# Kernel tuning notes

Measured on AMD Instinct MI355X. Metric: run time of the kernel, lower is better.

The kernel has to match this reference:

```python
import jax, jax.numpy as jnp
import numpy as np

N = 50000
E = 800000
DIM_IN = 128
DIM_H = 16
HEADS = 8
DIM_OUT = 16
NEG_SLOPE = 0.2


def setup_inputs() -> dict:
    key = jax.random.key(0)
    ks = jax.random.split(key, 12)
    def glorot(k, shape):
        fan_in = shape[0]
        return jax.random.normal(k, shape, dtype=jnp.float32) / np.sqrt(fan_in)
    x = jax.random.normal(ks[0], (N, DIM_IN), dtype=jnp.float32)
    edge_index = jax.random.randint(ks[1], (2, E), 0, N, dtype=jnp.int64)
    # layer 1: GATv2Conv(dim_in, dim_h, heads=8)
    Wl1 = glorot(ks[2], (DIM_IN, HEADS * DIM_H))
    Wr1 = glorot(ks[3], (DIM_IN, HEADS * DIM_H))
    att1 = glorot(ks[4], (HEADS, DIM_H))
    bias1 = jnp.zeros((HEADS * DIM_H,), dtype=jnp.float32)
    # layer 2: GATv2Conv(dim_h*heads, dim_out, heads=1)
    Wl2 = glorot(ks[5], (HEADS * DIM_H, DIM_OUT))
    Wr2 = glorot(ks[6], (HEADS * DIM_H, DIM_OUT))
    att2 = glorot(ks[7], (1, DIM_OUT))
    bias2 = jnp.zeros((DIM_OUT,), dtype=jnp.float32)
    return {"x": x, "edge_index": edge_index, "Wl1": Wl1, "Wr1": Wr1,
            "att1": att1, "bias1": bias1, "Wl2": Wl2, "Wr2": Wr2,
            "att2": att2, "bias2": bias2}


def gatv2_layer(x, src, dst, Wl, Wr, att, bias, n_nodes, heads, ch):
    # x: [N, F_in]; src/dst: [Etot] (self-loops included)
    xl = (x @ Wl).reshape(n_nodes, heads, ch)  # source transform
    xr = (x @ Wr).reshape(n_nodes, heads, ch)  # target transform
    e = jax.nn.leaky_relu(xl[src] + xr[dst], NEG_SLOPE)      # [Etot, H, C]
    logits = jnp.einsum('ehc,hc->eh', e, att)                # [Etot, H]
    # segment softmax over incoming edges of each target node
    m = jax.ops.segment_max(logits, dst, num_segments=n_nodes)
    a = jnp.exp(logits - m[dst])
    denom = jax.ops.segment_sum(a, dst, num_segments=n_nodes)
    alpha = a / denom[dst]                                   # [Etot, H]
    out = jax.ops.segment_sum(xl[src] * alpha[:, :, None], dst,
                              num_segments=n_nodes)          # [N, H, C]
    return out.reshape(n_nodes, heads * ch) + bias


def reference(x, edge_index, Wl1, Wr1, att1, bias1, Wl2, Wr2, att2, bias2):
    # PyG GATv2Conv adds self-loops by default
    loops = jnp.arange(N, dtype=edge_index.dtype)
    src = jnp.concatenate([edge_index[0], loops])
    dst = jnp.concatenate([edge_index[1], loops])
    # dropout is identity in eval mode
    h = gatv2_layer(x, src, dst, Wl1, Wr1, att1, bias1, N, HEADS, DIM_H)
    h = jax.nn.elu(h)
    h = gatv2_layer(h, src, dst, Wl2, Wr2, att2, bias2, N, 1, DIM_OUT)
    return h, jax.nn.log_softmax(h, axis=1)
```

## Files before the change

### kernel.cpp

```cpp
#include <hip/hip_runtime.h>
#include <hip/hip_bf16.h>
#include <math.h>

#define NN 50000
#define EE 800000
#define DIN 128
#define HEADS 8
#define DH 16
#define DOUT 16
#define NEG 0.2f
#define GM 32
#define GB ((NN + GM - 1) / GM)
#define NB ((NN + 255) / 256)
#define DEGB ((EE / 4 + 255) / 256)
#define NPART 8
#define RANGE (NN / NPART)
#define FILLB (DEGB * NPART)
#define PAD 64

typedef __attribute__((ext_vector_type(8))) short bf16x8;
typedef __attribute__((ext_vector_type(4))) float f32x4;
typedef __attribute__((ext_vector_type(4))) int i32x4;

__device__ __forceinline__ unsigned pack2bf(float a, float b) {
    union { __hip_bfloat162 h; unsigned u; } c;
    c.h = __float22bfloat162_rn(make_float2(a, b));
    return c.u;
}
__device__ __forceinline__ unsigned short f2bf(float v) {
    union { __hip_bfloat16 h; unsigned short u; } c;
    c.h = __float2bfloat16(v);
    return c.u;
}
__device__ __forceinline__ float bflo(unsigned u) { return __uint_as_float(u << 16); }
__device__ __forceinline__ float bfhi(unsigned u) { return __uint_as_float(u & 0xffff0000u); }

__global__ __launch_bounds__(256) void init_wcvt(int* __restrict__ cnt,
                                                 unsigned short* __restrict__ esrcPad,
                                                 const float* __restrict__ Wl,
                                                 const float* __restrict__ Wr,
                                                 unsigned short* __restrict__ Wb,
                                                 const float* __restrict__ Wl2,
                                                 const float* __restrict__ Wr2,
                                                 unsigned short* __restrict__ Wb2) {
    int b = blockIdx.x, t = threadIdx.x;
    if (b < NB) {
        int i = b * 256 + t;
        if (i < NN) {
            cnt[i] = 1;
            esrcPad[(size_t)i * PAD] = (unsigned short)i;
        }
    } else if (b < NB + 128) {
        int i = (b - NB) * 256 + t;
        int n = i >> 7, k = i & 127;
        float v = (n < 128) ? Wl[k * 128 + n] : Wr[k * 128 + (n - 128)];
        Wb[i] = f2bf(v);
    } else {
        int i = (b - NB - 128) * 256 + t;
        int n = i >> 7, k = i & 127;
        float v = (n < 16) ? Wl2[k * 16 + n] : Wr2[k * 16 + (n - 16)];
        Wb2[i] = f2bf(v);
    }
}

__global__ __launch_bounds__(256) void fill_gemm1(const int* __restrict__ ei,
                                                  int* __restrict__ cnt,
                                                  unsigned short* __restrict__ esrcPad,
                                                  const float* __restrict__ x,
                                                  const unsigned short* __restrict__ Wb,
                                                  unsigned short* __restrict__ xlb,
                                                  float* __restrict__ xr) {
    __shared__ unsigned short As[GM][136];
    int t = threadIdx.x;
    if (blockIdx.x < FILLB) {
        int chunk = blockIdx.x >> 3;
        int r = blockIdx.x & 7;
        int i = chunk * 256 + t;
        if (i >= EE / 4) return;
        i32x4 ss = __builtin_nontemporal_load(((const i32x4*)ei) + i);
        i32x4 dd = __builtin_nontemporal_load(((const i32x4*)(ei + EE)) + i);
        int lo = r * RANGE;
        int p;
        if ((unsigned)(dd[0] - lo) < RANGE) {
            p = atomicAdd(&cnt[dd[0]], 1);
            esrcPad[(size_t)dd[0] * PAD + p] = (unsigned short)ss[0];
        }
        if ((unsigned)(dd[1] - lo) < RANGE) {
            p = atomicAdd(&cnt[dd[1]], 1);
            esrcPad[(size_t)dd[1] * PAD + p] = (unsigned short)ss[1];
        }
        if ((unsigned)(dd[2] - lo) < RANGE) {
            p = atomicAdd(&cnt[dd[2]], 1);
            esrcPad[(size_t)dd[2] * PAD + p] = (unsigned short)ss[2];
        }
        if ((unsigned)(dd[3] - lo) < RANGE) {
            p = atomicAdd(&cnt[dd[3]], 1);
            esrcPad[(size_t)dd[3] * PAD + p] = (unsigned short)ss[3];
        }
        return;
    }
    int n0 = (blockIdx.x - FILLB) * GM;
    {
        int row = t >> 3, seg = t & 7;
        int nsrc = n0 + row < NN ? n0 + row : NN - 1;
        const f32x4* xp = (const f32x4*)(x + (size_t)nsrc * DIN + 16 * seg);
        f32x4 v0 = __builtin_nontemporal_load(xp);
        f32x4 v1 = __builtin_nontemporal_load(xp + 1);
        f32x4 v2 = __builtin_nontemporal_load(xp + 2);
        f32x4 v3 = __builtin_nontemporal_load(xp + 3);
        uint4 p0 = make_uint4(pack2bf(v0[0], v0[1]), pack2bf(v0[2], v0[3]),
                              pack2bf(v1[0], v1[1]), pack2bf(v1[2], v1[3]));
        uint4 p1 = make_uint4(pack2bf(v2[0], v2[1]), pack2bf(v2[2], v2[3]),
                              pack2bf(v3[0], v3[1]), pack2bf(v3[2], v3[3]));
        *(uint4*)&As[row][16 * seg]     = p0;
        *(uint4*)&As[row][16 * seg + 8] = p1;
    }
    __syncthreads();
    int lane = t & 63, w = t >> 6;
    int m = lane & 15, quad = lane >> 4;
    f32x4 acc[2][4];
#pragma unroll
    for (int mt = 0; mt < 2; ++mt)
#pragma unroll
        for (int nt = 0; nt < 4; ++nt) acc[mt][nt] = (f32x4){0.f, 0.f, 0.f, 0.f};
#pragma unroll
    for (int ks = 0; ks < 4; ++ks) {
        int k = 32 * ks + 8 * quad;
        bf16x8 a0 = *(const bf16x8*)&As[m][k];
        bf16x8 a1 = *(const bf16x8*)&As[16 + m][k];
#pragma unroll
        for (int nt = 0; nt < 4; ++nt) {
            int n = 64 * w + 16 * nt + m;
            bf16x8 b = *(const bf16x8*)(Wb + (size_t)n * 128 + k);
            acc[0][nt] = __builtin_amdgcn_mfma_f32_16x16x32_bf16(a0, b, acc[0][nt], 0, 0, 0);
            acc[1][nt] = __builtin_amdgcn_mfma_f32_16x16x32_bf16(a1, b, acc[1][nt], 0, 0, 0);
        }
    }
#pragma unroll
    for (int mt = 0; mt < 2; ++mt) {
#pragma unroll
        for (int nt = 0; nt < 4; ++nt) {
            int col = 64 * w + 16 * nt + m;
            int rbase = n0 + 16 * mt + 4 * quad;
            if (col < 128) {
#pragma unroll
                for (int r = 0; r < 4; ++r) {
                    int row = rbase + r;
                    if (row < NN) xlb[(size_t)row * DIN + col] = f2bf(acc[mt][nt][r]);
                }
            } else {
#pragma unroll
                for (int r = 0; r < 4; ++r) {
                    int row = rbase + r;
                    if (row < NN)
                        __builtin_nontemporal_store(acc[mt][nt][r],
                                                    &xr[(size_t)row * DIN + (col - 128)]);
                }
            }
        }
    }
}

__global__ __launch_bounds__(256) void l1_fused(const unsigned short* __restrict__ esrcPad,
                                                const int* __restrict__ cnt,
                                                const unsigned short* __restrict__ xlb,
                                                const float* __restrict__ xr,
                                                const float* __restrict__ att,
                                                const float* __restrict__ bias,
                                                unsigned short* __restrict__ hb) {
    int d = blockIdx.x * 4 + (threadIdx.x >> 6);
    int lane = threadIdx.x & 63;
    int quarter = lane >> 4;
    int q16 = lane & 15;
    int rs = d * PAD;
    int re = rs + cnt[d];
    int last = re - 1;
    float4 xr0 = ((const float4*)(xr + (size_t)d * DIN))[2 * q16];
    float4 xr1 = ((const float4*)(xr + (size_t)d * DIN))[2 * q16 + 1];
    float4 at0 = ((const float4*)att)[2 * q16];
    float4 at1 = ((const float4*)att)[2 * q16 + 1];
    float4 a0 = make_float4(0.f, 0.f, 0.f, 0.f);
    float4 a1 = make_float4(0.f, 0.f, 0.f, 0.f);
    float l = 0.f;
    int slot = rs + quarter;
    int c0 = slot < last ? slot : last;
    int s0 = esrcPad[c0];
    int c1 = slot + 4 < last ? slot + 4 : last;
    int s1 = esrcPad[c1];
    uint4 row = ((const uint4*)(xlb + (size_t)s0 * DIN))[q16];
    for (; slot < re; slot += 4) {
        uint4 cur = row;
        int c2 = slot + 8 < last ? slot + 8 : last;
        int s2 = esrcPad[c2];
        row = ((const uint4*)(xlb + (size_t)s1 * DIN))[q16];
        s1 = s2;
        float f0 = bflo(cur.x), f1 = bfhi(cur.x);
        float f2 = bflo(cur.y), f3 = bfhi(cur.y);
        float f4 = bflo(cur.z), f5 = bfhi(cur.z);
        float f6 = bflo(cur.w), f7 = bfhi(cur.w);
        float v0 = f0 + xr0.x; v0 = fmaxf(v0, NEG * v0);
        float v1 = f1 + xr0.y; v1 = fmaxf(v1, NEG * v1);
        float v2 = f2 + xr0.z; v2 = fmaxf(v2, NEG * v2);
        float v3 = f3 + xr0.w; v3 = fmaxf(v3, NEG * v3);
        float v4 = f4 + xr1.x; v4 = fmaxf(v4, NEG * v4);
        float v5 = f5 + xr1.y; v5 = fmaxf(v5, NEG * v5);
        float v6 = f6 + xr1.z; v6 = fmaxf(v6, NEG * v6);
        float v7 = f7 + xr1.w; v7 = fmaxf(v7, NEG * v7);
        float w = at0.x * v0 + at0.y * v1 + at0.z * v2 + at0.w * v3
                + at1.x * v4 + at1.y * v5 + at1.z * v6 + at1.w * v7;
        w += __shfl_xor(w, 1);
        float p = __expf(w);
        a0.x += p * f0; a0.y += p * f1; a0.z += p * f2; a0.w += p * f3;
        a1.x += p * f4; a1.y += p * f5; a1.z += p * f6; a1.w += p * f7;
        l += p;
    }
#pragma unroll
    for (int off = 16; off < 64; off <<= 1) {
        a0.x += __shfl_xor(a0.x, off); a0.y += __shfl_xor(a0.y, off);
        a0.z += __shfl_xor(a0.z, off); a0.w += __shfl_xor(a0.w, off);
        a1.x += __shfl_xor(a1.x, off); a1.y += __shfl_xor(a1.y, off);
        a1.z += __shfl_xor(a1.z, off); a1.w += __shfl_xor(a1.w, off);
        l += __shfl_xor(l, off);
    }
    if (quarter == 0) {
        float inv = 1.f / l;
        float4 b0 = ((const float4*)bias)[2 * q16];
        float4 b1 = ((const float4*)bias)[2 * q16 + 1];
        float4 o0, o1;
        o0.x = a0.x * inv + b0.x; o0.x = o0.x > 0.f ? o0.x : expm1f(o0.x);
        o0.y = a0.y * inv + b0.y; o0.y = o0.y > 0.f ? o0.y : expm1f(o0.y);
        o0.z = a0.z * inv + b0.z; o0.z = o0.z > 0.f ? o0.z : expm1f(o0.z);
        o0.w = a0.w * inv + b0.w; o0.w = o0.w > 0.f ? o0.w : expm1f(o0.w);
        o1.x = a1.x * inv + b1.x; o1.x = o1.x > 0.f ? o1.x : expm1f(o1.x);
        o1.y = a1.y * inv + b1.y; o1.y = o1.y > 0.f ? o1.y : expm1f(o1.y);
        o1.z = a1.z * inv + b1.z; o1.z = o1.z > 0.f ? o1.z : expm1f(o1.z);
        o1.w = a1.w * inv + b1.w; o1.w = o1.w > 0.f ? o1.w : expm1f(o1.w);
        uint4 pk = make_uint4(pack2bf(o0.x, o0.y), pack2bf(o0.z, o0.w),
                              pack2bf(o1.x, o1.y), pack2bf(o1.z, o1.w));
        ((uint4*)(hb + (size_t)d * DIN))[q16] = pk;
    }
}

__global__ __launch_bounds__(256) void gemm2(const unsigned short* __restrict__ hb,
                                             const unsigned short* __restrict__ Wb2,
                                             float* __restrict__ xl2, float* __restrict__ xr2) {
    __shared__ unsigned short As[GM][136];
    int t = threadIdx.x;
    int n0 = blockIdx.x * GM;
    {
        int row = t >> 3, s8 = t & 7;
        int nsrc = n0 + row < NN ? n0 + row : NN - 1;
        const uint4* src = (const uint4*)(hb + (size_t)nsrc * DIN);
        *(uint4*)&As[row][8 * s8]      = src[s8];
        *(uint4*)&As[row][8 * s8 + 64] = src[s8 + 8];
    }
    __syncthreads();
    int lane = t & 63, w = t >> 6;
    int m = lane & 15, quad = lane >> 4;
    int mt = w & 1, nt = w >> 1;
    f32x4 acc = (f32x4){0.f, 0.f, 0.f, 0.f};
#pragma unroll
    for (int ks = 0; ks < 4; ++ks) {
        int k = 32 * ks + 8 * quad;
        bf16x8 a = *(const bf16x8*)&As[16 * mt + m][k];
        bf16x8 b = *(const bf16x8*)(Wb2 + (size_t)(16 * nt + m) * 128 + k);
        acc = __builtin_amdgcn_mfma_f32_16x16x32_bf16(a, b, acc, 0, 0, 0);
    }
    float* __restrict__ dst = (nt == 0) ? xl2 : xr2;
#pragma unroll
    for (int r = 0; r < 4; ++r) {
        int node = n0 + 16 * mt + 4 * quad + r;
        if (node < NN) dst[(size_t)node * DOUT + m] = acc[r];
    }
}

__global__ __launch_bounds__(256) void l2_fused(const unsigned short* __restrict__ esrcPad,
                                                const int* __restrict__ cnt,
                                                const float* __restrict__ xl,
                                                const float* __restrict__ xr,
                                                const float* __restrict__ att,
                                                const float* __restrict__ bias,
                                                float* __restrict__ out) {
    int d = blockIdx.x * 4 + (threadIdx.x >> 6);
    int lane = threadIdx.x & 63;
    int sl = lane >> 2;
    int q = lane & 3;
    int rs = d * PAD;
    int re = rs + cnt[d];
    int last = re - 1;
    float4 xrq = ((const float4*)(xr + (size_t)d * DOUT))[q];
    float4 atq = ((const float4*)att)[q];
    float4 acc = make_float4(0.f, 0.f, 0.f, 0.f);
    float l = 0.f;
    int slot = rs + sl;
    int c0 = slot < last ? slot : last;
    int s0 = esrcPad[c0];
    for (; slot < re; slot += 16) {
        int c1 = slot + 16 < last ? slot + 16 : last;
        int s1 = esrcPad[c1];
        float4 cur = ((const float4*)(xl + (size_t)s0 * DOUT))[q];
        s0 = s1;
        float v0 = cur.x + xrq.x; v0 = fmaxf(v0, NEG * v0);
        float v1 = cur.y + xrq.y; v1 = fmaxf(v1, NEG * v1);
        float v2 = cur.z + xrq.z; v2 = fmaxf(v2, NEG * v2);
        float v3 = cur.w + xrq.w; v3 = fmaxf(v3, NEG * v3);
        float w = atq.x * v0 + atq.y * v1 + atq.z * v2 + atq.w * v3;
        w += __shfl_xor(w, 1);
        w += __shfl_xor(w, 2);
        float p = __expf(w);
        acc.x += p * cur.x; acc.y += p * cur.y;
        acc.z += p * cur.z; acc.w += p * cur.w;
        l += p;
    }
#pragma unroll
    for (int off = 4; off < 64; off <<= 1) {
        acc.x += __shfl_xor(acc.x, off);
        acc.y += __shfl_xor(acc.y, off);
        acc.z += __shfl_xor(acc.z, off);
        acc.w += __shfl_xor(acc.w, off);
        l += __shfl_xor(l, off);
    }
    float inv = 1.f / l;
    float4 b = ((const float4*)bias)[q];
    float4 v;
    v.x = acc.x * inv + b.x; v.y = acc.y * inv + b.y;
    v.z = acc.z * inv + b.z; v.w = acc.w * inv + b.w;
    float m = fmaxf(fmaxf(v.x, v.y), fmaxf(v.z, v.w));
    m = fmaxf(m, __shfl_xor(m, 1));
    m = fmaxf(m, __shfl_xor(m, 2));
    float es = __expf(v.x - m) + __expf(v.y - m) + __expf(v.z - m) + __expf(v.w - m);
    es += __shfl_xor(es, 1);
    es += __shfl_xor(es, 2);
    float lse = m + __logf(es);
    if (sl == 0) {
        ((float4*)(out + (size_t)d * DOUT))[q] = v;
        float4 ls;
        ls.x = v.x - lse; ls.y = v.y - lse; ls.z = v.z - lse; ls.w = v.w - lse;
        ((float4*)(out + (size_t)NN * DOUT + (size_t)d * DOUT))[q] = ls;
    }
}

extern "C" void kernel_launch(void* const* d_in, const int* in_sizes, int n_in,
                              void* d_out, int out_size, void* d_ws, size_t ws_size,
                              hipStream_t stream) {
    const float* x     = (const float*)d_in[0];
    const int*   ei    = (const int*)d_in[1];
    const float* Wl1   = (const float*)d_in[2];
    const float* Wr1   = (const float*)d_in[3];
    const float* att1  = (const float*)d_in[4];
    const float* bias1 = (const float*)d_in[5];
    const float* Wl2   = (const float*)d_in[6];
    const float* Wr2   = (const float*)d_in[7];
    const float* att2  = (const float*)d_in[8];
    const float* bias2 = (const float*)d_in[9];
    float* out = (float*)d_out;

    float* xr1    = (float*)d_ws;
    float* xl2    = xr1 + (size_t)NN * DIN;
    float* xr2    = xl2 + (size_t)NN * DOUT;
    unsigned short* xlb = (unsigned short*)(xr2 + (size_t)NN * DOUT);
    unsigned short* hb  = xlb + (size_t)NN * DIN;
    unsigned short* Wb  = hb + (size_t)NN * DIN;
    unsigned short* Wb2 = Wb + 256 * 128;
    unsigned short* esrcPad = Wb2 + 32 * 128;
    int*   cnt    = (int*)(esrcPad + (size_t)NN * PAD);

    const int B = 256;
    init_wcvt<<<NB + 144, B, 0, stream>>>(cnt, esrcPad, Wl1, Wr1, Wb, Wl2, Wr2, Wb2);
    fill_gemm1<<<FILLB + GB, B, 0, stream>>>(ei, cnt, esrcPad, x, Wb, xlb, xr1);

    l1_fused<<<NN / 4, B, 0, stream>>>(esrcPad, cnt, xlb, xr1, att1, bias1, hb);

    gemm2<<<GB, B, 0, stream>>>(hb, Wb2, xl2, xr2);

    l2_fused<<<NN / 4, B, 0, stream>>>(esrcPad, cnt, xl2, xr2, att2, bias2, out);
}
```

Baseline: 237.9 us.

## Store layer-1 features head-major and split aggregation per head

Layer-1 source and target features, and the hidden output, are now stored head-major ([head][node][16]) instead of node-major. The aggregation kernel launches one block group per head, so each wave handles 8 edges at a time with 8 lanes per edge, and each gathered row is only 32 bytes per head. The likely aim is to shrink each gathered working set to one head's slice so it fits better in cache, and to raise parallelism. In exchange, every edge index is read eight times, the gathers are narrower, and gemm2 must reassemble rows from eight separate head planes.

```diff
diff --git a/kernel.cpp b/kernel.cpp
--- a/kernel.cpp
+++ b/kernel.cpp
@@ -20,6 +20,7 @@
 
 typedef __attribute__((ext_vector_type(8))) short bf16x8;
 typedef __attribute__((ext_vector_type(4))) float f32x4;
+typedef __attribute__((ext_vector_type(2))) float f32x2;
 typedef __attribute__((ext_vector_type(4))) int i32x4;
 
 __device__ __forceinline__ unsigned pack2bf(float a, float b) {
@@ -140,21 +141,24 @@
     for (int mt = 0; mt < 2; ++mt) {
 #pragma unroll
         for (int nt = 0; nt < 4; ++nt) {
-            int col = 64 * w + 16 * nt + m;
             int rbase = n0 + 16 * mt + 4 * quad;
-            if (col < 128) {
+            if (w < 2) {
+                int h = 4 * w + nt;
 #pragma unroll
                 for (int r = 0; r < 4; ++r) {
                     int row = rbase + r;
-                    if (row < NN) xlb[(size_t)row * DIN + col] = f2bf(acc[mt][nt][r]);
+                    if (row < NN)
+                        __builtin_nontemporal_store(f2bf(acc[mt][nt][r]),
+                            &xlb[((size_t)h * NN + row) * 16 + m]);
                 }
             } else {
+                int h = 4 * (w - 2) + nt;
 #pragma unroll
                 for (int r = 0; r < 4; ++r) {
                     int row = rbase + r;
                     if (row < NN)
                         __builtin_nontemporal_store(acc[mt][nt][r],
-                                                    &xr[(size_t)row * DIN + (col - 128)]);
+                            &xr[((size_t)h * NN + row) * 16 + m]);
                 }
             }
         }
@@ -168,76 +172,49 @@
                                                 const float* __restrict__ att,
                                                 const float* __restrict__ bias,
                                                 unsigned short* __restrict__ hb) {
-    int d = blockIdx.x * 4 + (threadIdx.x >> 6);
+    int h = blockIdx.x & 7;
+    int d = (blockIdx.x >> 3) * 4 + (threadIdx.x >> 6);
     int lane = threadIdx.x & 63;
-    int quarter = lane >> 4;
-    int q16 = lane & 15;
+    int e  = lane >> 3;
+    int c2 = lane & 7;
+    const unsigned short* xlbH = xlb + (size_t)h * NN * 16;
+    const float* xrH = xr + (size_t)h * NN * 16;
+    f32x2 xrv = __builtin_nontemporal_load(((const f32x2*)(xrH + (size_t)d * 16)) + c2);
+    float2 atv = ((const float2*)(att + (size_t)h * 16))[c2];
     int rs = d * PAD;
     int re = rs + cnt[d];
     int last = re - 1;
-    float4 xr0 = ((const float4*)(xr + (size_t)d * DIN))[2 * q16];
-    float4 xr1 = ((const float4*)(xr + (size_t)d * DIN))[2 * q16 + 1];
-    float4 at0 = ((const float4*)att)[2 * q16];
-    float4 at1 = ((const float4*)att)[2 * q16 + 1];
-    float4 a0 = make_float4(0.f, 0.f, 0.f, 0.f);
-    float4 a1 = make_float4(0.f, 0.f, 0.f, 0.f);
-    float l = 0.f;
-    int slot = rs + quarter;
-    int c0 = slot < last ? slot : last;
-    int s0 = esrcPad[c0];
-    int c1 = slot + 4 < last ? slot + 4 : last;
-    int s1 = esrcPad[c1];
-    uint4 row = ((const uint4*)(xlb + (size_t)s0 * DIN))[q16];
-    for (; slot < re; slot += 4) {
-        uint4 cur = row;
-        int c2 = slot + 8 < last ? slot + 8 : last;
-        int s2 = esrcPad[c2];
-        row = ((const uint4*)(xlb + (size_t)s1 * DIN))[q16];
-        s1 = s2;
-        float f0 = bflo(cur.x), f1 = bfhi(cur.x);
-        float f2 = bflo(cur.y), f3 = bfhi(cur.y);
-        float f4 = bflo(cur.z), f5 = bfhi(cur.z);
-        float f6 = bflo(cur.w), f7 = bfhi(cur.w);
-        float v0 = f0 + xr0.x; v0 = fmaxf(v0, NEG * v0);
-        float v1 = f1 + xr0.y; v1 = fmaxf(v1, NEG * v1);
-        float v2 = f2 + xr0.z; v2 = fmaxf(v2, NEG * v2);
-        float v3 = f3 + xr0.w; v3 = fmaxf(v3, NEG * v3);
-        float v4 = f4 + xr1.x; v4 = fmaxf(v4, NEG * v4);
-        float v5 = f5 + xr1.y; v5 = fmaxf(v5, NEG * v5);
-        float v6 = f6 + xr1.z; v6 = fmaxf(v6, NEG * v6);
-        float v7 = f7 + xr1.w; v7 = fmaxf(v7, NEG * v7);
-        float w = at0.x * v0 + at0.y * v1 + at0.z * v2 + at0.w * v3
-                + at1.x * v4 + at1.y * v5 + at1.z * v6 + at1.w * v7;
+    float acc0 = 0.f, acc1 = 0.f, l = 0.f;
+    int slot = rs + e;
+    int ci = slot < last ? slot : last;
+    int s0 = __builtin_nontemporal_load(&esrcPad[ci]);
+    for (; slot < re; slot += 8) {
+        int ni = slot + 8 < last ? slot + 8 : last;
+        int s1 = __builtin_nontemporal_load(&esrcPad[ni]);
+        unsigned u = ((const unsigned*)(xlbH + (size_t)s0 * 16))[c2];
+        s0 = s1;
+        float f0 = bflo(u), f1 = bfhi(u);
+        float v0 = f0 + xrv[0]; v0 = fmaxf(v0, NEG * v0);
+        float v1 = f1 + xrv[1]; v1 = fmaxf(v1, NEG * v1);
+        float w = atv.x * v0 + atv.y * v1;
         w += __shfl_xor(w, 1);
+        w += __shfl_xor(w, 2);
+        w += __shfl_xor(w, 4);
         float p = __expf(w);
-        a0.x += p * f0; a0.y += p * f1; a0.z += p * f2; a0.w += p * f3;
-        a1.x += p * f4; a1.y += p * f5; a1.z += p * f6; a1.w += p * f7;
-        l += p;
-    }
-#pragma unroll
-    for (int off = 16; off < 64; off <<= 1) {
-        a0.x += __shfl_xor(a0.x, off); a0.y += __shfl_xor(a0.y, off);
-        a0.z += __shfl_xor(a0.z, off); a0.w += __shfl_xor(a0.w, off);
-        a1.x += __shfl_xor(a1.x, off); a1.y += __shfl_xor(a1.y, off);
-        a1.z += __shfl_xor(a1.z, off); a1.w += __shfl_xor(a1.w, off);
-        l += __shfl_xor(l, off);
-    }
-    if (quarter == 0) {
+        acc0 += p * f0; acc1 += p * f1; l += p;
+    }
+#pragma unroll
+    for (int off = 8; off < 64; off <<= 1) {
+        acc0 += __shfl_xor(acc0, off);
+        acc1 += __shfl_xor(acc1, off);
+        l    += __shfl_xor(l, off);
+    }
+    if (e == 0) {
         float inv = 1.f / l;
-        float4 b0 = ((const float4*)bias)[2 * q16];
-        float4 b1 = ((const float4*)bias)[2 * q16 + 1];
-        float4 o0, o1;
-        o0.x = a0.x * inv + b0.x; o0.x = o0.x > 0.f ? o0.x : expm1f(o0.x);
-        o0.y = a0.y * inv + b0.y; o0.y = o0.y > 0.f ? o0.y : expm1f(o0.y);
-        o0.z = a0.z * inv + b0.z; o0.z = o0.z > 0.f ? o0.z : expm1f(o0.z);
-        o0.w = a0.w * inv + b0.w; o0.w = o0.w > 0.f ? o0.w : expm1f(o0.w);
-        o1.x = a1.x * inv + b1.x; o1.x = o1.x > 0.f ? o1.x : expm1f(o1.x);
-        o1.y = a1.y * inv + b1.y; o1.y = o1.y > 0.f ? o1.y : expm1f(o1.y);
-        o1.z = a1.z * inv + b1.z; o1.z = o1.z > 0.f ? o1.z : expm1f(o1.z);
-        o1.w = a1.w * inv + b1.w; o1.w = o1.w > 0.f ? o1.w : expm1f(o1.w);
-        uint4 pk = make_uint4(pack2bf(o0.x, o0.y), pack2bf(o0.z, o0.w),
-                              pack2bf(o1.x, o1.y), pack2bf(o1.z, o1.w));
-        ((uint4*)(hb + (size_t)d * DIN))[q16] = pk;
+        float2 bs = ((const float2*)(bias + (size_t)h * 16))[c2];
+        float o0 = acc0 * inv + bs.x; o0 = o0 > 0.f ? o0 : expm1f(o0);
+        float o1 = acc1 * inv + bs.y; o1 = o1 > 0.f ? o1 : expm1f(o1);
+        ((unsigned*)(hb + ((size_t)h * NN + d) * 16))[c2] = pack2bf(o0, o1);
     }
 }
 
@@ -248,11 +225,11 @@
     int t = threadIdx.x;
     int n0 = blockIdx.x * GM;
     {
-        int row = t >> 3, s8 = t & 7;
+        int s8 = t >> 5, row = t & 31;
         int nsrc = n0 + row < NN ? n0 + row : NN - 1;
-        const uint4* src = (const uint4*)(hb + (size_t)nsrc * DIN);
-        *(uint4*)&As[row][8 * s8]      = src[s8];
-        *(uint4*)&As[row][8 * s8 + 64] = src[s8 + 8];
+        const uint4* src = (const uint4*)(hb + ((size_t)s8 * NN + nsrc) * 16);
+        *(uint4*)&As[row][16 * s8]     = src[0];
+        *(uint4*)&As[row][16 * s8 + 8] = src[1];
     }
     __syncthreads();
     int lane = t & 63, w = t >> 6;
@@ -369,7 +346,7 @@
     init_wcvt<<<NB + 144, B, 0, stream>>>(cnt, esrcPad, Wl1, Wr1, Wb, Wl2, Wr2, Wb2);
     fill_gemm1<<<FILLB + GB, B, 0, stream>>>(ei, cnt, esrcPad, x, Wb, xlb, xr1);
 
-    l1_fused<<<NN / 4, B, 0, stream>>>(esrcPad, cnt, xlb, xr1, att1, bias1, hb);
+    l1_fused<<<(NN / 4) * 8, B, 0, stream>>>(esrcPad, cnt, xlb, xr1, att1, bias1, hb);
 
     gemm2<<<GB, B, 0, stream>>>(hb, Wb2, xl2, xr2);
 
```

Measured after the change: 383.0 us. 61.0% more time.
